# Optimization experiments

Measured on AMD Instinct MI355X. Metric: run time of the kernel, lower is better.

Reference implementation:

```python
import jax, jax.numpy as jnp
import numpy as np
import math

WIDTH = 1024
DATA_WIDTH = 1024
HEADS = 16


def setup_inputs() -> dict:
    key = jax.random.key(0)
    ks = jax.random.split(key, 8)
    bs, n_ctx, n_data = 2, 1024, 4096
    init_scale = 0.25 / math.sqrt(WIDTH)
    inp = {
        "x": jax.random.normal(ks[0], (bs, n_ctx, WIDTH), dtype=jnp.float32),
        "data": jax.random.normal(ks[1], (bs, n_data, DATA_WIDTH), dtype=jnp.float32),
        "Wq": jax.random.normal(ks[2], (WIDTH, WIDTH), dtype=jnp.float32) * init_scale,
        "bq": jnp.zeros((WIDTH,), dtype=jnp.float32),
        "Wkv": jax.random.normal(ks[3], (DATA_WIDTH, 2 * WIDTH), dtype=jnp.float32) * init_scale,
        "bkv": jnp.zeros((2 * WIDTH,), dtype=jnp.float32),
        "Wproj": jax.random.normal(ks[4], (WIDTH, WIDTH), dtype=jnp.float32) * init_scale,
        "bproj": jnp.zeros((WIDTH,), dtype=jnp.float32),
    }
    return inp


def reference(x, data, Wq, bq, Wkv, bkv, Wproj, bproj):
    bs, n_ctx, _ = x.shape
    _, n_data, _ = data.shape
    h = HEADS
    attn_ch = WIDTH // h  # = (2*width)//heads//2
    scale = 1.0 / math.sqrt(math.sqrt(attn_ch))

    q = x @ Wq + bq                      # [bs, n_ctx, width]
    kv = data @ Wkv + bkv                # [bs, n_data, 2*width]

    q = q.reshape(bs, n_ctx, h, attn_ch)
    kv = kv.reshape(bs, n_data, h, 2 * attn_ch)
    k, v = kv[..., :attn_ch], kv[..., attn_ch:]

    # full O(n_ctx * n_data) attention weights, softmax in fp32 (faithful to use_flash=False path)
    weight = jnp.einsum('bthc,bshc->bhts', q * scale, k * scale)
    wdtype = weight.dtype
    weight = jax.nn.softmax(weight.astype(jnp.float32), axis=-1).astype(wdtype)
    out = jnp.einsum('bhts,bshc->bthc', weight, v).reshape(bs, n_ctx, WIDTH)

    return out @ Wproj + bproj
```

## Files before the change

kernel.cpp:

```cpp
#include <hip/hip_runtime.h>
#include <hip/hip_bf16.h>


typedef __bf16 bf16;
typedef float f32x4 __attribute__((ext_vector_type(4)));
typedef bf16 bf16x8 __attribute__((ext_vector_type(8)));

#define MFMA16(A, B, C) __builtin_amdgcn_mfma_f32_16x16x32_bf16((A), (B), (C), 0, 0, 0)

constexpr int BS = 2;
constexpr int NCTX = 1024;
constexpr int NDATA = 4096;
constexpr int WID = 1024;
constexpr int NH = 16;
constexpr int DH = 64;
constexpr int NSPLIT = 4;
constexpr float ATT_SCALE = 0.35355339059327373f;

__device__ __forceinline__ void gload16(const void* g, void* l) {
  __builtin_amdgcn_global_load_lds(
      (const __attribute__((address_space(1))) unsigned int*)g,
      (__attribute__((address_space(3))) unsigned int*)l, 16, 0, 0);
}

__global__ __launch_bounds__(256) void prep_kernel(
    const float* __restrict__ x, const float* __restrict__ data,
    const float* __restrict__ Wq, const float* __restrict__ Wkv,
    const float* __restrict__ Wproj, bf16* __restrict__ x16,
    bf16* __restrict__ d16, bf16* __restrict__ wqT, bf16* __restrict__ wkvT,
    bf16* __restrict__ wprojT) {
  __shared__ float tile[64][65];
  const int bid = blockIdx.x, tid = threadIdx.x;
  if (bid < 5120) {
    const float* src;
    bf16* dst;
    size_t i;
    if (bid < 1024) {
      src = x; dst = x16; i = ((size_t)bid * 256 + tid) * 8;
    } else {
      src = data; dst = d16; i = ((size_t)(bid - 1024) * 256 + tid) * 8;
    }
    float4 v0 = *reinterpret_cast<const float4*>(&src[i]);
    float4 v1 = *reinterpret_cast<const float4*>(&src[i + 4]);
    bf16x8 o;
    o[0] = (bf16)v0.x; o[1] = (bf16)v0.y; o[2] = (bf16)v0.z; o[3] = (bf16)v0.w;
    o[4] = (bf16)v1.x; o[5] = (bf16)v1.y; o[6] = (bf16)v1.z; o[7] = (bf16)v1.w;
    *reinterpret_cast<bf16x8*>(&dst[i]) = o;
    return;
  }
  const int t = bid - 5120;
  const float* in;
  bf16* out;
  int R = 1024, C, cx, ry;
  if (t < 256) {
    in = Wq; out = wqT; C = 1024; cx = t & 15; ry = t >> 4;
  } else if (t < 768) {
    int u = t - 256; in = Wkv; out = wkvT; C = 2048; cx = u & 31; ry = u >> 5;
  } else {
    int u = t - 768; in = Wproj; out = wprojT; C = 1024; cx = u & 15; ry = u >> 4;
  }
  const int c0 = cx * 64, r0 = ry * 64;
#pragma unroll
  for (int i = 0; i < 16; ++i) {
    int idx = tid + i * 256;
    int row = idx >> 6, col = idx & 63;
    tile[row][col] = in[(size_t)(r0 + row) * C + (c0 + col)];
  }
  __syncthreads();
#pragma unroll
  for (int i = 0; i < 16; ++i) {
    int idx = tid + i * 256;
    int orow = idx >> 6, ocol = idx & 63;
    out[(size_t)(c0 + orow) * R + (r0 + ocol)] = (bf16)tile[ocol][orow];
  }
}

#define GEMM64x128_LOOP(Aptr, Bptr)                                            \
  __shared__ bf16 As[64][32];                                                  \
  __shared__ bf16 Bs[128][32];                                                 \
  const int tid = threadIdx.x, lane = tid & 63, w = tid >> 6;                  \
  const int wm = (w & 1) * 32, wn = (w >> 1) * 64;                             \
  const int l15 = lane & 15, l4 = lane >> 4;                                   \
  const int sr = lane >> 2, sc = (lane & 3) * 8;                               \
  const bf16* a_s = (Aptr) + (((size_t)(m0 + w * 16 + sr)) << 10) + sc;        \
  const bf16* b_s0 = (Bptr) + (((size_t)(n0 + w * 32 + sr)) << 10) + sc;       \
  const bf16* b_s1 = (Bptr) + (((size_t)(n0 + w * 32 + 16 + sr)) << 10) + sc;  \
  f32x4 acc[2][4] = {};                                                        \
  for (int kt = 0; kt < 32; ++kt) {                                            \
    __syncthreads();                                                           \
    gload16(a_s + kt * 32, &As[w * 16][0]);                                    \
    gload16(b_s0 + kt * 32, &Bs[w * 32][0]);                                   \
    gload16(b_s1 + kt * 32, &Bs[w * 32 + 16][0]);                              \
    __syncthreads();                                                           \
    bf16x8 af[2], bfr[4];                                                      \
    _Pragma("unroll") for (int mi = 0; mi < 2; ++mi)                           \
        af[mi] = *reinterpret_cast<const bf16x8*>(&As[wm + mi * 16 + l15][l4 * 8]); \
    _Pragma("unroll") for (int ni = 0; ni < 4; ++ni)                           \
        bfr[ni] = *reinterpret_cast<const bf16x8*>(&Bs[wn + ni * 16 + l15][l4 * 8]); \
    _Pragma("unroll") for (int mi = 0; mi < 2; ++mi)                           \
        _Pragma("unroll") for (int ni = 0; ni < 4; ++ni)                       \
            acc[mi][ni] = MFMA16(af[mi], bfr[ni], acc[mi][ni]);                \
  }

__global__ __launch_bounds__(256) void gemm_q_kernel(
    const bf16* __restrict__ X, const bf16* __restrict__ WT,
    const float* __restrict__ bias, bf16* __restrict__ Q) {
  const int nt = blockIdx.x & 7, mt = blockIdx.x >> 3;
  const int m0 = mt * 64, n0 = nt * 128;
  GEMM64x128_LOOP(X, WT)
#pragma unroll
  for (int ni = 0; ni < 4; ++ni) {
    int n = n0 + wn + ni * 16 + l15;
    float bv = bias[n];
    int h = n >> 6, d = n & 63;
#pragma unroll
    for (int mi = 0; mi < 2; ++mi)
#pragma unroll
      for (int r = 0; r < 4; ++r) {
        int m = m0 + wm + mi * 16 + l4 * 4 + r;
        int b = m >> 10, t = m & 1023;
        Q[(((size_t)(b * NH + h)) * NCTX + t) * DH + d] =
            (bf16)((acc[mi][ni][r] + bv) * ATT_SCALE);
      }
  }
}

__global__ __launch_bounds__(256) void gemm_proj_kernel(
    const bf16* __restrict__ A, const bf16* __restrict__ WT,
    const float* __restrict__ bias, float* __restrict__ OUT) {
  const int nt = blockIdx.x & 7, mt = blockIdx.x >> 3;
  const int m0 = mt * 64, n0 = nt * 128;
  GEMM64x128_LOOP(A, WT)
#pragma unroll
  for (int ni = 0; ni < 4; ++ni) {
    int n = n0 + wn + ni * 16 + l15;
    float bv = bias[n];
#pragma unroll
    for (int mi = 0; mi < 2; ++mi)
#pragma unroll
      for (int r = 0; r < 4; ++r) {
        int m = m0 + wm + mi * 16 + l4 * 4 + r;
        OUT[(size_t)m * 1024 + n] = acc[mi][ni][r] + bv;
      }
  }
}

__global__ __launch_bounds__(512) void gemm_kv_kernel(
    const bf16* __restrict__ DATA,
    const bf16* __restrict__ WT,
    const float* __restrict__ bias,
    bf16* __restrict__ Kb,
    bf16* __restrict__ Vt) {
  __shared__ bf16 As[2][2][128][64];
  __shared__ bf16 Bs[2][2][128][64];
  const int tid = threadIdx.x, lane = tid & 63, w = tid >> 6;
  const int l15 = lane & 15, l4 = lane >> 4;
  const int wg = (blockIdx.x & 7) * 32 + (blockIdx.x >> 3);
  const int nt = wg & 7, mt = wg >> 3;
  const int m0 = mt * 256, n0 = nt * 256;
  const int wr = w >> 2, wc = w & 3;

  const int rA = tid >> 3;
  const int cgs = ((tid & 7) ^ (rA & 7)) << 3;
  const bf16* a_src0 = DATA + (((size_t)(m0 + rA)) << 10) + cgs;
  const bf16* a_src1 = DATA + (((size_t)(m0 + 128 + rA)) << 10) + cgs;
  const bf16* b_src0 = WT + (((size_t)(n0 + rA)) << 10) + cgs;
  const bf16* b_src1 = WT + (((size_t)(n0 + 128 + rA)) << 10) + cgs;

#define STAGE_A(t_, d_)                                                  \
  gload16(a_src0 + (t_) * 64, &As[d_][0][8 * w][0]);                     \
  gload16(a_src0 + (t_) * 64 + (64 << 10), &As[d_][0][64 + 8 * w][0]);   \
  gload16(a_src1 + (t_) * 64, &As[d_][1][8 * w][0]);                     \
  gload16(a_src1 + (t_) * 64 + (64 << 10), &As[d_][1][64 + 8 * w][0]);
#define STAGE_B(t_, d_)                                                  \
  gload16(b_src0 + (t_) * 64, &Bs[d_][0][8 * w][0]);                     \
  gload16(b_src0 + (t_) * 64 + (64 << 10), &Bs[d_][0][64 + 8 * w][0]);   \
  gload16(b_src1 + (t_) * 64, &Bs[d_][1][8 * w][0]);                     \
  gload16(b_src1 + (t_) * 64 + (64 << 10), &Bs[d_][1][64 + 8 * w][0]);

  const int sw = (l15 & 7) << 4;
  const int koff0 = (((l4 << 4)) ^ sw) >> 1;
  const int koff1 = ((64 + (l4 << 4)) ^ sw) >> 1;
  const bf16* Arow = &As[0][wr][l15][0];
  const bf16* Brow = &Bs[0][wc >> 1][(wc & 1) * 64 + l15][0];
  const int dstrideA = 2 * 128 * 64;

#define LDA(d_, mi, koff_) \
  (*reinterpret_cast<const bf16x8*>(Arow + (d_) * dstrideA + (mi) * 1024 + (koff_)))
#define LDB(d_, ni, koff_) \
  (*reinterpret_cast<const bf16x8*>(Brow + (d_) * dstrideA + (ni) * 1024 + (koff_)))

  f32x4 acc[8][4] = {};

  STAGE_A(0, 0)
  STAGE_B(0, 0)

  for (int t = 0; t < 16; ++t) {
    const int d = t & 1;
    if (t < 15) {
      STAGE_A(t + 1, d ^ 1)
      asm volatile("s_waitcnt vmcnt(4)" ::: "memory");
    } else {
      asm volatile("s_waitcnt vmcnt(0)" ::: "memory");
    }
    __builtin_amdgcn_s_barrier();
    asm volatile("" ::: "memory");
    if (t < 15) { STAGE_B(t + 1, d ^ 1) }
    bf16x8 bf00 = LDB(d, 0, koff0), bf01 = LDB(d, 0, koff1);
    bf16x8 bf10 = LDB(d, 1, koff0), bf11 = LDB(d, 1, koff1);
    bf16x8 bf20 = LDB(d, 2, koff0), bf21 = LDB(d, 2, koff1);
    bf16x8 bf30 = LDB(d, 3, koff0), bf31 = LDB(d, 3, koff1);
#pragma unroll
    for (int p = 0; p < 4; ++p) {
      bf16x8 a00 = LDA(d, 2 * p, koff0), a01 = LDA(d, 2 * p, koff1);
      bf16x8 a10 = LDA(d, 2 * p + 1, koff0), a11 = LDA(d, 2 * p + 1, koff1);
      __builtin_amdgcn_s_setprio(1);
      acc[2 * p][0] = MFMA16(a00, bf00, acc[2 * p][0]);
      acc[2 * p][0] = MFMA16(a01, bf01, acc[2 * p][0]);
      acc[2 * p][1] = MFMA16(a00, bf10, acc[2 * p][1]);
      acc[2 * p][1] = MFMA16(a01, bf11, acc[2 * p][1]);
      acc[2 * p][2] = MFMA16(a00, bf20, acc[2 * p][2]);
      acc[2 * p][2] = MFMA16(a01, bf21, acc[2 * p][2]);
      acc[2 * p][3] = MFMA16(a00, bf30, acc[2 * p][3]);
      acc[2 * p][3] = MFMA16(a01, bf31, acc[2 * p][3]);
      acc[2 * p + 1][0] = MFMA16(a10, bf00, acc[2 * p + 1][0]);
      acc[2 * p + 1][0] = MFMA16(a11, bf01, acc[2 * p + 1][0]);
      acc[2 * p + 1][1] = MFMA16(a10, bf10, acc[2 * p + 1][1]);
      acc[2 * p + 1][1] = MFMA16(a11, bf11, acc[2 * p + 1][1]);
      acc[2 * p + 1][2] = MFMA16(a10, bf20, acc[2 * p + 1][2]);
      acc[2 * p + 1][2] = MFMA16(a11, bf21, acc[2 * p + 1][2]);
      acc[2 * p + 1][3] = MFMA16(a10, bf30, acc[2 * p + 1][3]);
      acc[2 * p + 1][3] = MFMA16(a11, bf31, acc[2 * p + 1][3]);
      __builtin_amdgcn_s_setprio(0);
    }
    asm volatile("" ::: "memory");
    __builtin_amdgcn_s_barrier();
  }
#undef STAGE_A
#undef STAGE_B
#undef LDA
#undef LDB

#pragma unroll
  for (int ni = 0; ni < 4; ++ni) {
    int n = n0 + wc * 64 + ni * 16 + l15;
    float bv = bias[n];
    int h = n >> 7, c = n & 127;
#pragma unroll
    for (int mi = 0; mi < 8; ++mi)
#pragma unroll
      for (int r = 0; r < 4; ++r) {
        int m = m0 + wr * 128 + mi * 16 + l4 * 4 + r;
        int b = m >> 12, s = m & 4095;
        float vv = acc[mi][ni][r] + bv;
        if (c < DH) {
          Kb[(((size_t)(b * NH + h)) * NDATA + s) * DH + c] = (bf16)(vv * ATT_SCALE);
        } else {
          Vt[(((size_t)(b * NH + h)) * DH + (c - DH)) * NDATA + s] = (bf16)vv;
        }
      }
  }
}

__global__ __launch_bounds__(256) void attn_kernel(
    const bf16* __restrict__ Q,
    const bf16* __restrict__ Kb,
    const bf16* __restrict__ Vt,
    bf16* __restrict__ Op,
    float* __restrict__ Ls) {
  constexpr int SCH = 32;
  constexpr int NIT = (NDATA / NSPLIT) / SCH;
  __shared__ bf16 Ks[2][32][64];
  __shared__ bf16 Vs[2][64][32];
  const int tid = threadIdx.x, lane = tid & 63, w = tid >> 6;
  const int wg = (blockIdx.x & 7) * 256 + (blockIdx.x >> 3);
  const int tt = wg & 15, sp = (wg >> 4) & 3, h = (wg >> 6) & 15, b = wg >> 10;
  const int t0 = tt * 64 + w * 16;
  const int l15 = lane & 15, l4 = lane >> 4;
  const size_t qbase = (((size_t)(b * NH + h)) * NCTX + t0) * DH;
  const size_t kbase = ((size_t)(b * NH + h)) * NDATA * DH;
  const size_t vbase = ((size_t)(b * NH + h)) * DH * NDATA;

  bf16x8 qf0 = *reinterpret_cast<const bf16x8*>(&Q[qbase + (size_t)l15 * DH + l4 * 8]);
  bf16x8 qf1 = *reinterpret_cast<const bf16x8*>(&Q[qbase + (size_t)l15 * DH + 32 + l4 * 8]);

  const int krow0 = ((l15 >> 2) << 3) + (l15 & 3);
  const int kf_swz = ((l15 & 3) | (((l15 >> 2) & 1) << 2)) << 4;
  const int koff_a = ((l4 * 16) ^ kf_swz) >> 1;
  const int koff_b = ((64 + l4 * 16) ^ kf_swz) >> 1;
  const int voff = ((l4 * 16) ^ ((l15 & 3) << 4)) >> 1;

  const int kst_off = (w * 8 + (lane >> 3)) * 128 +
      (((lane & 7) * 16) ^ (((((lane >> 3) & 3)) | ((w & 1) << 2)) << 4));
  const int vrow_g = w * 16 + (lane >> 2);
  const char* vrowp = (const char*)(Vt + vbase + (size_t)vrow_g * NDATA);
  const int vst_coff = ((lane & 3) * 16) ^ ((((lane >> 2) & 3)) << 4);
  const char* kchunk = (const char*)(Kb + kbase);

  f32x4 o[4] = {};
  float lsum = 0.f;

  const int sstart = sp * (NDATA / NSPLIT);
  gload16(kchunk + (size_t)sstart * 128 + kst_off, &Ks[0][w * 8][0]);
  gload16(vrowp + (size_t)sstart * 2 + vst_coff, &Vs[0][w * 16][0]);
  __syncthreads();

  int cur = 0;
  for (int it = 0; it < NIT; ++it) {
    const int s0 = sstart + it * SCH;
    if (it + 1 < NIT) {
      gload16(kchunk + (size_t)(s0 + SCH) * 128 + kst_off, &Ks[cur ^ 1][w * 8][0]);
      gload16(vrowp + (size_t)(s0 + SCH) * 2 + vst_coff, &Vs[cur ^ 1][w * 16][0]);
    }
    f32x4 p0 = {}, p1 = {};
    {
      bf16x8 a00 = *reinterpret_cast<const bf16x8*>(&Ks[cur][krow0][koff_a]);
      bf16x8 a01 = *reinterpret_cast<const bf16x8*>(&Ks[cur][krow0][koff_b]);
      p0 = MFMA16(a00, qf0, p0);
      p0 = MFMA16(a01, qf1, p0);
      bf16x8 a10 = *reinterpret_cast<const bf16x8*>(&Ks[cur][krow0 + 4][koff_a]);
      bf16x8 a11 = *reinterpret_cast<const bf16x8*>(&Ks[cur][krow0 + 4][koff_b]);
      p1 = MFMA16(a10, qf0, p1);
      p1 = MFMA16(a11, qf1, p1);
    }
    bf16x8 paf;
#pragma unroll
    for (int r = 0; r < 4; ++r) {
      float e = __expf(p0[r]);
      lsum += e;
      paf[r] = (bf16)e;
    }
#pragma unroll
    for (int r = 0; r < 4; ++r) {
      float e = __expf(p1[r]);
      lsum += e;
      paf[4 + r] = (bf16)e;
    }
#pragma unroll
    for (int dg = 0; dg < 4; ++dg) {
      bf16x8 vf = *reinterpret_cast<const bf16x8*>(&Vs[cur][dg * 16 + l15][voff]);
      o[dg] = MFMA16(paf, vf, o[dg]);
    }
    __syncthreads();
    cur ^= 1;
  }

  const size_t obase = (((size_t)((sp * BS + b) * NH + h)) * NCTX + t0);
  lsum += __shfl_xor(lsum, 16, 64);
  lsum += __shfl_xor(lsum, 32, 64);
  if (l4 == 0) Ls[obase + l15] = lsum;
#pragma unroll
  for (int dg = 0; dg < 4; ++dg)
#pragma unroll
    for (int r = 0; r < 4; ++r)
      Op[(obase + l4 * 4 + r) * DH + dg * 16 + l15] = (bf16)o[dg][r];
}

__global__ __launch_bounds__(256) void attn_combine_kernel(
    const bf16* __restrict__ Op, const float* __restrict__ Ls,
    bf16* __restrict__ AO) {
  const int idx = blockIdx.x * 256 + threadIdx.x;
  const int d = idx & 63;
  const int t = (idx >> 6) & (NCTX - 1);
  const int h = (idx >> 16) & (NH - 1);
  const int b = idx >> 20;
  float os = 0.f, ls = 0.f;
#pragma unroll
  for (int p = 0; p < NSPLIT; ++p) {
    size_t base = ((size_t)((p * BS + b) * NH + h)) * NCTX + t;
    os += (float)Op[base * DH + d];
    ls += Ls[base];
  }
  AO[((size_t)b * NCTX + t) * WID + h * DH + d] = (bf16)(os / ls);
}

extern "C" void kernel_launch(void* const* d_in, const int* in_sizes, int n_in,
                              void* d_out, int out_size, void* d_ws, size_t ws_size,
                              hipStream_t stream) {
  const float* x = (const float*)d_in[0];
  const float* data = (const float*)d_in[1];
  const float* Wq = (const float*)d_in[2];
  const float* bq = (const float*)d_in[3];
  const float* Wkv = (const float*)d_in[4];
  const float* bkv = (const float*)d_in[5];
  const float* Wproj = (const float*)d_in[6];
  const float* bproj = (const float*)d_in[7];
  float* out = (float*)d_out;

  char* ws = (char*)d_ws;
  size_t off = 0;
  auto alloc = [&](size_t bytes) -> void* {
    void* p = ws + off;
    off += (bytes + 255) & ~(size_t)255;
    return p;
  };
  bf16* d16 = (bf16*)alloc((size_t)BS * NDATA * WID * 2);
  bf16* x16 = (bf16*)alloc((size_t)BS * NCTX * WID * 2);
  bf16* qbuf = (bf16*)alloc((size_t)BS * NH * NCTX * DH * 2);
  bf16* kbuf = (bf16*)alloc((size_t)BS * NH * NDATA * DH * 2);
  bf16* vt = (bf16*)alloc((size_t)BS * NH * DH * NDATA * 2);
  bf16* wqT = (bf16*)alloc((size_t)WID * WID * 2);
  bf16* wkvT = (bf16*)alloc((size_t)2 * WID * WID * 2);
  bf16* wprojT = (bf16*)alloc((size_t)WID * WID * 2);
  float* lsbuf = (float*)alloc((size_t)NSPLIT * BS * NH * NCTX * 4);
  bf16* opbuf = d16;
  bf16* aobuf = x16;

  prep_kernel<<<dim3(6144), 256, 0, stream>>>(x, data, Wq, Wkv, Wproj,
                                              x16, d16, wqT, wkvT, wprojT);
  gemm_q_kernel<<<dim3(256), 256, 0, stream>>>(x16, wqT, bq, qbuf);
  gemm_kv_kernel<<<dim3(256), 512, 0, stream>>>(d16, wkvT, bkv, kbuf, vt);
  attn_kernel<<<dim3(BS * NH * (NCTX / 64) * NSPLIT), 256, 0, stream>>>(
      qbuf, kbuf, vt, opbuf, lsbuf);
  attn_combine_kernel<<<dim3(BS * NCTX * WID / 256), 256, 0, stream>>>(opbuf, lsbuf, aobuf);
  gemm_proj_kernel<<<dim3(256), 256, 0, stream>>>(aobuf, wprojT, bproj, out);
}
```

Measured before the change: 256.9 us.

## Enlarge attention tile to 32 query rows per wave and 64-key chunks, use exp2

Each wave now handles 32 query rows instead of 16 and each iteration stages 64 keys instead of 32. Every K/V fragment read from LDS is reused across two query sub-tiles, and there are half as many barriers per key. The log2(e) factor is folded into the Q scaling so the softmax can call exp2f directly, and MFMA sections get raised wave priority. The costs are more registers (occupancy hint of 3 blocks per CU), twice the LDS, and half as many blocks in the grid.

```diff
diff --git a/kernel.cpp b/kernel.cpp
--- a/kernel.cpp
+++ b/kernel.cpp
@@ -16,6 +16,7 @@
 constexpr int DH = 64;
 constexpr int NSPLIT = 4;
 constexpr float ATT_SCALE = 0.35355339059327373f;
+constexpr float QSCALE = ATT_SCALE * 1.4426950408889634f;
 
 __device__ __forceinline__ void gload16(const void* g, void* l) {
   __builtin_amdgcn_global_load_lds(
@@ -120,7 +121,7 @@
         int m = m0 + wm + mi * 16 + l4 * 4 + r;
         int b = m >> 10, t = m & 1023;
         Q[(((size_t)(b * NH + h)) * NCTX + t) * DH + d] =
-            (bf16)((acc[mi][ni][r] + bv) * ATT_SCALE);
+            (bf16)((acc[mi][ni][r] + bv) * QSCALE);
       }
   }
 }
@@ -262,98 +263,126 @@
   }
 }
 
-__global__ __launch_bounds__(256) void attn_kernel(
+__global__ __launch_bounds__(256, 3) void attn_kernel(
     const bf16* __restrict__ Q,
     const bf16* __restrict__ Kb,
     const bf16* __restrict__ Vt,
     bf16* __restrict__ Op,
     float* __restrict__ Ls) {
-  constexpr int SCH = 32;
+  constexpr int SCH = 64;
   constexpr int NIT = (NDATA / NSPLIT) / SCH;
-  __shared__ bf16 Ks[2][32][64];
-  __shared__ bf16 Vs[2][64][32];
+  __shared__ bf16 Ks[2][64][64];
+  __shared__ bf16 Vs[2][64][64];
   const int tid = threadIdx.x, lane = tid & 63, w = tid >> 6;
-  const int wg = (blockIdx.x & 7) * 256 + (blockIdx.x >> 3);
-  const int tt = wg & 15, sp = (wg >> 4) & 3, h = (wg >> 6) & 15, b = wg >> 10;
-  const int t0 = tt * 64 + w * 16;
+  const int wg = (blockIdx.x & 7) * 128 + (blockIdx.x >> 3);
+  const int tt = wg & 7, sp = (wg >> 3) & 3, h = (wg >> 5) & 15, b = wg >> 9;
+  const int t0 = tt * 128 + w * 32;
   const int l15 = lane & 15, l4 = lane >> 4;
   const size_t qbase = (((size_t)(b * NH + h)) * NCTX + t0) * DH;
   const size_t kbase = ((size_t)(b * NH + h)) * NDATA * DH;
   const size_t vbase = ((size_t)(b * NH + h)) * DH * NDATA;
 
-  bf16x8 qf0 = *reinterpret_cast<const bf16x8*>(&Q[qbase + (size_t)l15 * DH + l4 * 8]);
-  bf16x8 qf1 = *reinterpret_cast<const bf16x8*>(&Q[qbase + (size_t)l15 * DH + 32 + l4 * 8]);
+  bf16x8 qf[2][2];
+#pragma unroll
+  for (int m = 0; m < 2; ++m) {
+    qf[m][0] = *reinterpret_cast<const bf16x8*>(&Q[qbase + (size_t)(m * 16 + l15) * DH + l4 * 8]);
+    qf[m][1] = *reinterpret_cast<const bf16x8*>(&Q[qbase + (size_t)(m * 16 + l15) * DH + 32 + l4 * 8]);
+  }
 
   const int krow0 = ((l15 >> 2) << 3) + (l15 & 3);
   const int kf_swz = ((l15 & 3) | (((l15 >> 2) & 1) << 2)) << 4;
   const int koff_a = ((l4 * 16) ^ kf_swz) >> 1;
   const int koff_b = ((64 + l4 * 16) ^ kf_swz) >> 1;
-  const int voff = ((l4 * 16) ^ ((l15 & 3) << 4)) >> 1;
-
-  const int kst_off = (w * 8 + (lane >> 3)) * 128 +
-      (((lane & 7) * 16) ^ (((((lane >> 3) & 3)) | ((w & 1) << 2)) << 4));
-  const int vrow_g = w * 16 + (lane >> 2);
-  const char* vrowp = (const char*)(Vt + vbase + (size_t)vrow_g * NDATA);
-  const int vst_coff = ((lane & 3) * 16) ^ ((((lane >> 2) & 3)) << 4);
-  const char* kchunk = (const char*)(Kb + kbase);
-
-  f32x4 o[4] = {};
-  float lsum = 0.f;
+  const int voff0 = ((l4 * 16) ^ ((l15 & 7) << 4)) >> 1;
+  const int voff1 = ((64 + l4 * 16) ^ ((l15 & 7) << 4)) >> 1;
+
+  const int rk = lane >> 3, sl = lane & 7;
+  const bf16* kp = Kb + kbase + (size_t)(8 * w + rk) * 64 +
+                   (sl ^ ((rk & 3) | ((w & 1) << 2))) * 8;
+  const bf16* vp = Vt + vbase + (size_t)(8 * w + rk) * NDATA + (sl ^ rk) * 8;
+
+  f32x4 o[2][4] = {};
+  f32x4 lacc[2] = {};
 
   const int sstart = sp * (NDATA / NSPLIT);
-  gload16(kchunk + (size_t)sstart * 128 + kst_off, &Ks[0][w * 8][0]);
-  gload16(vrowp + (size_t)sstart * 2 + vst_coff, &Vs[0][w * 16][0]);
+
+#define STAGE(buf_, s0_)                                                   \
+  gload16(kp + (size_t)(s0_) * 64, &Ks[buf_][8 * w][0]);                   \
+  gload16(kp + (size_t)(s0_) * 64 + 2048, &Ks[buf_][32 + 8 * w][0]);       \
+  gload16(vp + (s0_), &Vs[buf_][8 * w][0]);                                \
+  gload16(vp + (s0_) + (size_t)32 * NDATA, &Vs[buf_][32 + 8 * w][0]);
+
+  STAGE(0, sstart)
   __syncthreads();
 
   int cur = 0;
   for (int it = 0; it < NIT; ++it) {
     const int s0 = sstart + it * SCH;
-    if (it + 1 < NIT) {
-      gload16(kchunk + (size_t)(s0 + SCH) * 128 + kst_off, &Ks[cur ^ 1][w * 8][0]);
-      gload16(vrowp + (size_t)(s0 + SCH) * 2 + vst_coff, &Vs[cur ^ 1][w * 16][0]);
+    if (it + 1 < NIT) { STAGE(cur ^ 1, s0 + SCH) }
+    bf16x8 ka[2][2][2];
+#pragma unroll
+    for (int sh = 0; sh < 2; ++sh)
+#pragma unroll
+      for (int sg = 0; sg < 2; ++sg) {
+        const bf16* kr = &Ks[cur][32 * sh + krow0 + 4 * sg][0];
+        ka[sh][sg][0] = *reinterpret_cast<const bf16x8*>(kr + koff_a);
+        ka[sh][sg][1] = *reinterpret_cast<const bf16x8*>(kr + koff_b);
+      }
+    bf16x8 paf[2][2];
+#pragma unroll
+    for (int m = 0; m < 2; ++m) {
+      f32x4 p00 = {}, p01 = {}, p10 = {}, p11 = {};
+      __builtin_amdgcn_s_setprio(1);
+      p00 = MFMA16(ka[0][0][0], qf[m][0], p00);
+      p00 = MFMA16(ka[0][0][1], qf[m][1], p00);
+      p01 = MFMA16(ka[0][1][0], qf[m][0], p01);
+      p01 = MFMA16(ka[0][1][1], qf[m][1], p01);
+      p10 = MFMA16(ka[1][0][0], qf[m][0], p10);
+      p10 = MFMA16(ka[1][0][1], qf[m][1], p10);
+      p11 = MFMA16(ka[1][1][0], qf[m][0], p11);
+      p11 = MFMA16(ka[1][1][1], qf[m][1], p11);
+      __builtin_amdgcn_s_setprio(0);
+#pragma unroll
+      for (int r = 0; r < 4; ++r) {
+        float e0 = exp2f(p00[r]), e1 = exp2f(p01[r]);
+        float e2 = exp2f(p10[r]), e3 = exp2f(p11[r]);
+        lacc[m][r] += (e0 + e1) + (e2 + e3);
+        paf[m][0][r] = (bf16)e0;
+        paf[m][0][4 + r] = (bf16)e1;
+        paf[m][1][r] = (bf16)e2;
+        paf[m][1][4 + r] = (bf16)e3;
+      }
     }
-    f32x4 p0 = {}, p1 = {};
-    {
-      bf16x8 a00 = *reinterpret_cast<const bf16x8*>(&Ks[cur][krow0][koff_a]);
-      bf16x8 a01 = *reinterpret_cast<const bf16x8*>(&Ks[cur][krow0][koff_b]);
-      p0 = MFMA16(a00, qf0, p0);
-      p0 = MFMA16(a01, qf1, p0);
-      bf16x8 a10 = *reinterpret_cast<const bf16x8*>(&Ks[cur][krow0 + 4][koff_a]);
-      bf16x8 a11 = *reinterpret_cast<const bf16x8*>(&Ks[cur][krow0 + 4][koff_b]);
-      p1 = MFMA16(a10, qf0, p1);
-      p1 = MFMA16(a11, qf1, p1);
-    }
-    bf16x8 paf;
-#pragma unroll
-    for (int r = 0; r < 4; ++r) {
-      float e = __expf(p0[r]);
-      lsum += e;
-      paf[r] = (bf16)e;
-    }
-#pragma unroll
-    for (int r = 0; r < 4; ++r) {
-      float e = __expf(p1[r]);
-      lsum += e;
-      paf[4 + r] = (bf16)e;
-    }
 #pragma unroll
     for (int dg = 0; dg < 4; ++dg) {
-      bf16x8 vf = *reinterpret_cast<const bf16x8*>(&Vs[cur][dg * 16 + l15][voff]);
-      o[dg] = MFMA16(paf, vf, o[dg]);
+      const bf16* vr = &Vs[cur][dg * 16 + l15][0];
+      bf16x8 vf0 = *reinterpret_cast<const bf16x8*>(vr + voff0);
+      bf16x8 vf1 = *reinterpret_cast<const bf16x8*>(vr + voff1);
+      __builtin_amdgcn_s_setprio(1);
+      o[0][dg] = MFMA16(paf[0][0], vf0, o[0][dg]);
+      o[0][dg] = MFMA16(paf[0][1], vf1, o[0][dg]);
+      o[1][dg] = MFMA16(paf[1][0], vf0, o[1][dg]);
+      o[1][dg] = MFMA16(paf[1][1], vf1, o[1][dg]);
+      __builtin_amdgcn_s_setprio(0);
     }
     __syncthreads();
     cur ^= 1;
   }
-
-  const size_t obase = (((size_t)((sp * BS + b) * NH + h)) * NCTX + t0);
-  lsum += __shfl_xor(lsum, 16, 64);
-  lsum += __shfl_xor(lsum, 32, 64);
-  if (l4 == 0) Ls[obase + l15] = lsum;
-#pragma unroll
-  for (int dg = 0; dg < 4; ++dg)
-#pragma unroll
-    for (int r = 0; r < 4; ++r)
-      Op[(obase + l4 * 4 + r) * DH + dg * 16 + l15] = (bf16)o[dg][r];
+#undef STAGE
+
+#pragma unroll
+  for (int m = 0; m < 2; ++m) {
+    float ls = (lacc[m][0] + lacc[m][1]) + (lacc[m][2] + lacc[m][3]);
+    ls += __shfl_xor(ls, 16, 64);
+    ls += __shfl_xor(ls, 32, 64);
+    const size_t obase = (((size_t)((sp * BS + b) * NH + h)) * NCTX + t0 + m * 16);
+    if (l4 == 0) Ls[obase + l15] = ls;
+#pragma unroll
+    for (int dg = 0; dg < 4; ++dg)
+#pragma unroll
+      for (int r = 0; r < 4; ++r)
+        Op[(obase + l4 * 4 + r) * DH + dg * 16 + l15] = (bf16)o[m][dg][r];
+  }
 }
 
 __global__ __launch_bounds__(256) void attn_combine_kernel(
@@ -410,7 +439,7 @@
                                               x16, d16, wqT, wkvT, wprojT);
   gemm_q_kernel<<<dim3(256), 256, 0, stream>>>(x16, wqT, bq, qbuf);
   gemm_kv_kernel<<<dim3(256), 512, 0, stream>>>(d16, wkvT, bkv, kbuf, vt);
-  attn_kernel<<<dim3(BS * NH * (NCTX / 64) * NSPLIT), 256, 0, stream>>>(
+  attn_kernel<<<dim3(BS * NH * (NCTX / 128) * NSPLIT), 256, 0, stream>>>(
       qbuf, kbuf, vt, opbuf, lsbuf);
   attn_combine_kernel<<<dim3(BS * NCTX * WID / 256), 256, 0, stream>>>(opbuf, lsbuf, aobuf);
   gemm_proj_kernel<<<dim3(256), 256, 0, stream>>>(aobuf, wprojT, bproj, out);
```

Result: faster. 249.0 us (-3.1%).
